# Optimization experiments

Hardware: AMD Instinct MI355X
Metric: run time of the kernel (lower is better)

## Reference

```python
import jax, jax.numpy as jnp
import numpy as np

N_NODES = 20000
N_EDGES = 640000
IN_DIM = 128
HID = 128
OUT_DIM = 3
N_GRAPHS = 32


def setup_inputs() -> dict:
    key = jax.random.key(0)
    ks = jax.random.split(key, 12)
    x = jax.random.normal(ks[0], (N_NODES, IN_DIM), dtype=jnp.float32)
    edge_index = jax.random.randint(ks[1], (2, N_EDGES), 0, N_NODES, dtype=jnp.int64)
    batch = jnp.sort(jax.random.randint(ks[2], (N_NODES,), 0, N_GRAPHS, dtype=jnp.int64))
    batch = batch.at[0].set(0).at[-1].set(N_GRAPHS - 1)
    s = 0.05
    W_gcn = jax.random.normal(ks[3], (IN_DIM, HID), jnp.float32) * s
    b_gcn = jnp.zeros((HID,), jnp.float32)
    W_sage_l = jax.random.normal(ks[4], (HID, HID), jnp.float32) * s  # neighbor branch
    W_sage_r = jax.random.normal(ks[5], (HID, HID), jnp.float32) * s  # root branch
    b_sage = jnp.zeros((HID,), jnp.float32)
    W_fc1 = jax.random.normal(ks[6], (HID, HID), jnp.float32) * s
    b_fc1 = jnp.zeros((HID,), jnp.float32)
    W_fc2 = jax.random.normal(ks[7], (HID, OUT_DIM), jnp.float32) * s
    b_fc2 = jnp.zeros((OUT_DIM,), jnp.float32)
    return {
        'x': x, 'edge_index': edge_index, 'batch': batch,
        'W_gcn': W_gcn, 'b_gcn': b_gcn,
        'W_sage_l': W_sage_l, 'W_sage_r': W_sage_r, 'b_sage': b_sage,
        'W_fc1': W_fc1, 'b_fc1': b_fc1, 'W_fc2': W_fc2, 'b_fc2': b_fc2,
    }


def reference(x, edge_index, batch, W_gcn, b_gcn, W_sage_l, W_sage_r, b_sage,
              W_fc1, b_fc1, W_fc2, b_fc2):
    n = x.shape[0]
    row, col = edge_index[0], edge_index[1]  # source -> target

    # ---- GCNConv: symmetric-normalized aggregation with self-loops ----
    h = x @ W_gcn  # [N, H]
    loops = jnp.arange(n, dtype=row.dtype)
    row_sl = jnp.concatenate([row, loops])
    col_sl = jnp.concatenate([col, loops])
    deg = jax.ops.segment_sum(jnp.ones_like(col_sl, dtype=h.dtype), col_sl,
                              num_segments=n)
    dinv = jnp.where(deg > 0, jax.lax.rsqrt(deg), 0.0)
    norm = dinv[row_sl] * dinv[col_sl]  # [E+N]
    h_gcn = jax.ops.segment_sum(h[row_sl] * norm[:, None], col_sl,
                                num_segments=n) + b_gcn
    h_gcn = jax.nn.relu(h_gcn)

    # ---- SAGEConv (mean aggregator) ----
    cnt = jax.ops.segment_sum(jnp.ones_like(col, dtype=h_gcn.dtype), col,
                              num_segments=n)
    neigh = jax.ops.segment_sum(h_gcn[row], col, num_segments=n)
    neigh = neigh / jnp.maximum(cnt, 1.0)[:, None]
    h_sage = neigh @ W_sage_l + h_gcn @ W_sage_r + b_sage
    h_sage = jax.nn.relu(h_sage)

    # ---- global_add_pool (num_graphs = 32 < 50) ----
    pooled = jax.ops.segment_sum(h_sage, batch, num_segments=N_GRAPHS)  # [G, H]

    # ---- MLP head ----
    out = jax.nn.relu(pooled @ W_fc1 + b_fc1) @ W_fc2 + b_fc2  # [G, 3]
    return out
```

## Files before the change

### kernel.cpp

```cpp
#include <hip/hip_runtime.h>

#define N_NODES 20000
#define N_EDGES 640000
#define HID 128
#define N_GRAPHS 32

#define SCAN_BLK 256
#define SCAN_NBLK ((N_NODES + SCAN_BLK - 1) / SCAN_BLK)

#define XT_STRIDE 36

__global__ __launch_bounds__(256) void hist_k(const int* __restrict__ col,
                                              int* __restrict__ cnt) {
    int e = blockIdx.x * blockDim.x + threadIdx.x;
    if (e < N_EDGES) {
        int c = col[e];
        if ((unsigned)c < N_NODES) atomicAdd(&cnt[c], 1);
    }
}

__global__ __launch_bounds__(SCAN_BLK) void scanA_k(const int* __restrict__ cnt,
                                                    int* __restrict__ blkSum) {
    __shared__ int wsum[SCAN_BLK / 64];
    const int b = blockIdx.x, t = threadIdx.x;
    const int i = b * SCAN_BLK + t;
    int v = (i < N_NODES) ? cnt[i] : 0;
#pragma unroll
    for (int o = 1; o < 64; o <<= 1) v += __shfl_xor(v, o);
    if ((t & 63) == 0) wsum[t >> 6] = v;
    __syncthreads();
    if (t == 0) {
        int s = 0;
#pragma unroll
        for (int w = 0; w < SCAN_BLK / 64; ++w) s += wsum[w];
        blkSum[b] = s;
    }
}

__global__ __launch_bounds__(SCAN_BLK) void scanB_k(const int* __restrict__ cnt,
                                                    const int* __restrict__ blkSum,
                                                    int* __restrict__ offs,
                                                    int* __restrict__ cursor,
                                                    float* __restrict__ dinv) {
    __shared__ int sm[SCAN_BLK];
    __shared__ int base_s;
    const int b = blockIdx.x, t = threadIdx.x;
    const int i = b * SCAN_BLK + t;
    const int v = (i < N_NODES) ? cnt[i] : 0;
    sm[t] = v;
    if (t == 0) {
        int s = 0;
        for (int k = 0; k < b; ++k) s += blkSum[k];
        base_s = s;
    }
    __syncthreads();
    for (int o = 1; o < SCAN_BLK; o <<= 1) {
        int add = (t >= o) ? sm[t - o] : 0;
        __syncthreads();
        sm[t] += add;
        __syncthreads();
    }
    if (i < N_NODES) {
        int excl = base_s + ((t > 0) ? sm[t - 1] : 0);
        offs[i] = excl;
        cursor[i] = excl;
        dinv[i] = rsqrtf((float)(v + 1));
        if (i == N_NODES - 1) offs[N_NODES] = excl + v;
    }
}

__global__ __launch_bounds__(256) void fill_k(const int* __restrict__ row,
                                              const int* __restrict__ col,
                                              int* __restrict__ cursor,
                                              int* __restrict__ csr_src) {
    int e = blockIdx.x * blockDim.x + threadIdx.x;
    if (e < N_EDGES) {
        int c = col[e];
        int r = row[e];
        if ((unsigned)c < N_NODES && (unsigned)r < N_NODES) {
            int p = atomicAdd(&cursor[c], 1);
            csr_src[p] = r;
        }
    }
}

__device__ __forceinline__ void stage_xt(float* xt, const float* __restrict__ Xm,
                                         int row0, int t) {
    const int r = t & 31;
    const int kbase = (t >> 5) * 16;
    const float* xp = Xm + (size_t)(row0 + r) * 128 + kbase;
#pragma unroll
    for (int c = 0; c < 4; ++c) {
        float4 v = *(const float4*)&xp[c * 4];
        xt[(kbase + c * 4 + 0) * XT_STRIDE + r] = v.x;
        xt[(kbase + c * 4 + 1) * XT_STRIDE + r] = v.y;
        xt[(kbase + c * 4 + 2) * XT_STRIDE + r] = v.z;
        xt[(kbase + c * 4 + 3) * XT_STRIDE + r] = v.w;
    }
}

__device__ __forceinline__ void gemm_half(const float* xt, const float* wbuf,
                                          int kb, int rg, int c4, float4 acc[4]) {
#pragma unroll 8
    for (int k0 = 0; k0 < 64; ++k0) {
        float4 w = *(const float4*)&wbuf[k0 * 128 + c4];
        float4 xr = *(const float4*)&xt[(kb + k0) * XT_STRIDE + rg * 4];
        acc[0].x = fmaf(xr.x, w.x, acc[0].x);
        acc[0].y = fmaf(xr.x, w.y, acc[0].y);
        acc[0].z = fmaf(xr.x, w.z, acc[0].z);
        acc[0].w = fmaf(xr.x, w.w, acc[0].w);
        acc[1].x = fmaf(xr.y, w.x, acc[1].x);
        acc[1].y = fmaf(xr.y, w.y, acc[1].y);
        acc[1].z = fmaf(xr.y, w.z, acc[1].z);
        acc[1].w = fmaf(xr.y, w.w, acc[1].w);
        acc[2].x = fmaf(xr.z, w.x, acc[2].x);
        acc[2].y = fmaf(xr.z, w.y, acc[2].y);
        acc[2].z = fmaf(xr.z, w.z, acc[2].z);
        acc[2].w = fmaf(xr.z, w.w, acc[2].w);
        acc[3].x = fmaf(xr.w, w.x, acc[3].x);
        acc[3].y = fmaf(xr.w, w.y, acc[3].y);
        acc[3].z = fmaf(xr.w, w.z, acc[3].z);
        acc[3].w = fmaf(xr.w, w.w, acc[3].w);
    }
}

__global__ __launch_bounds__(256) void gemm128_k(const float* __restrict__ X,
                                                 const float* __restrict__ W,
                                                 float* __restrict__ Y) {
    __shared__ float wbuf[64 * 128];
    __shared__ float xt[128 * XT_STRIDE];
    const int t = threadIdx.x;
    const int rg = t >> 5;
    const int c4 = (t & 31) * 4;
    const int row0 = blockIdx.x * 32;
    float4 acc[4];
    acc[0] = acc[1] = acc[2] = acc[3] = make_float4(0.f, 0.f, 0.f, 0.f);
    stage_xt(xt, X, row0, t);
#pragma unroll
    for (int kc = 0; kc < 2; ++kc) {
        if (kc) __syncthreads();
#pragma unroll
        for (int i = 0; i < 8; ++i)
            ((float4*)wbuf)[t + i * 256] = ((const float4*)W)[kc * 2048 + t + i * 256];
        __syncthreads();
        gemm_half(xt, wbuf, kc * 64, rg, c4, acc);
    }
#pragma unroll
    for (int i = 0; i < 4; ++i)
        *(float4*)&Y[(size_t)(row0 + rg * 4 + i) * 128 + c4] = acc[i];
}

__global__ __launch_bounds__(256) void gcn_agg_k(const float* __restrict__ h,
                                                 const int* __restrict__ offs,
                                                 const int* __restrict__ src,
                                                 const float* __restrict__ dinv,
                                                 const float* __restrict__ bias,
                                                 float* __restrict__ out) {
    const int wave = threadIdx.x >> 6;
    const int lane = threadIdx.x & 63;
    const int half = lane >> 5;
    const int node = (blockIdx.x * 4 + wave) * 2 + half;
    const int c4 = (lane & 31) * 4;
    const int nd = (node < N_NODES) ? node : (N_NODES - 1);
    const float dc = dinv[nd];
    float4 hv = *(const float4*)&h[(size_t)nd * 128 + c4];
    float4 acc = make_float4(dc * hv.x, dc * hv.y, dc * hv.z, dc * hv.w);
    const int beg = offs[nd];
    const int deg = offs[nd + 1] - beg;
    const int mdeg = max(deg, __shfl(deg, lane ^ 32));
    for (int j = 0; j < mdeg; j += 4) {
        int i0 = (j + 0 < deg) ? beg + j + 0 : 0;
        int i1 = (j + 1 < deg) ? beg + j + 1 : 0;
        int i2 = (j + 2 < deg) ? beg + j + 2 : 0;
        int i3 = (j + 3 < deg) ? beg + j + 3 : 0;
        int s0 = src[i0], s1 = src[i1], s2 = src[i2], s3 = src[i3];
        float w0 = (j + 0 < deg) ? dinv[s0] : 0.f;
        float w1 = (j + 1 < deg) ? dinv[s1] : 0.f;
        float w2 = (j + 2 < deg) ? dinv[s2] : 0.f;
        float w3 = (j + 3 < deg) ? dinv[s3] : 0.f;
        float4 v0 = *(const float4*)&h[(size_t)s0 * 128 + c4];
        float4 v1 = *(const float4*)&h[(size_t)s1 * 128 + c4];
        float4 v2 = *(const float4*)&h[(size_t)s2 * 128 + c4];
        float4 v3 = *(const float4*)&h[(size_t)s3 * 128 + c4];
        acc.x = fmaf(w0, v0.x, fmaf(w1, v1.x, fmaf(w2, v2.x, fmaf(w3, v3.x, acc.x))));
        acc.y = fmaf(w0, v0.y, fmaf(w1, v1.y, fmaf(w2, v2.y, fmaf(w3, v3.y, acc.y))));
        acc.z = fmaf(w0, v0.z, fmaf(w1, v1.z, fmaf(w2, v2.z, fmaf(w3, v3.z, acc.z))));
        acc.w = fmaf(w0, v0.w, fmaf(w1, v1.w, fmaf(w2, v2.w, fmaf(w3, v3.w, acc.w))));
    }
    float4 b = *(const float4*)&bias[c4];
    float4 o;
    o.x = fmaxf(fmaf(dc, acc.x, b.x), 0.f);
    o.y = fmaxf(fmaf(dc, acc.y, b.y), 0.f);
    o.z = fmaxf(fmaf(dc, acc.z, b.z), 0.f);
    o.w = fmaxf(fmaf(dc, acc.w, b.w), 0.f);
    if (node < N_NODES) *(float4*)&out[(size_t)node * 128 + c4] = o;
}

__global__ __launch_bounds__(256) void sage_agg_k(const float* __restrict__ hg,
                                                  const int* __restrict__ offs,
                                                  const int* __restrict__ src,
                                                  float* __restrict__ out) {
    const int wave = threadIdx.x >> 6;
    const int lane = threadIdx.x & 63;
    const int half = lane >> 5;
    const int node = (blockIdx.x * 4 + wave) * 2 + half;
    const int c4 = (lane & 31) * 4;
    const int nd = (node < N_NODES) ? node : (N_NODES - 1);
    float4 acc = make_float4(0.f, 0.f, 0.f, 0.f);
    const int beg = offs[nd];
    const int deg = offs[nd + 1] - beg;
    const int mdeg = max(deg, __shfl(deg, lane ^ 32));
    for (int j = 0; j < mdeg; j += 4) {
        int i0 = (j + 0 < deg) ? beg + j + 0 : 0;
        int i1 = (j + 1 < deg) ? beg + j + 1 : 0;
        int i2 = (j + 2 < deg) ? beg + j + 2 : 0;
        int i3 = (j + 3 < deg) ? beg + j + 3 : 0;
        float w0 = (j + 0 < deg) ? 1.f : 0.f;
        float w1 = (j + 1 < deg) ? 1.f : 0.f;
        float w2 = (j + 2 < deg) ? 1.f : 0.f;
        float w3 = (j + 3 < deg) ? 1.f : 0.f;
        int s0 = src[i0], s1 = src[i1], s2 = src[i2], s3 = src[i3];
        float4 v0 = *(const float4*)&hg[(size_t)s0 * 128 + c4];
        float4 v1 = *(const float4*)&hg[(size_t)s1 * 128 + c4];
        float4 v2 = *(const float4*)&hg[(size_t)s2 * 128 + c4];
        float4 v3 = *(const float4*)&hg[(size_t)s3 * 128 + c4];
        acc.x = fmaf(w0, v0.x, fmaf(w1, v1.x, fmaf(w2, v2.x, fmaf(w3, v3.x, acc.x))));
        acc.y = fmaf(w0, v0.y, fmaf(w1, v1.y, fmaf(w2, v2.y, fmaf(w3, v3.y, acc.y))));
        acc.z = fmaf(w0, v0.z, fmaf(w1, v1.z, fmaf(w2, v2.z, fmaf(w3, v3.z, acc.z))));
        acc.w = fmaf(w0, v0.w, fmaf(w1, v1.w, fmaf(w2, v2.w, fmaf(w3, v3.w, acc.w))));
    }
    float inv = 1.0f / (float)max(deg, 1);
    float4 o;
    o.x = acc.x * inv;
    o.y = acc.y * inv;
    o.z = acc.z * inv;
    o.w = acc.w * inv;
    if (node < N_NODES) *(float4*)&out[(size_t)node * 128 + c4] = o;
}

__global__ __launch_bounds__(256) void combine_k(const float* __restrict__ An,
                                                 const float* __restrict__ Bh,
                                                 const float* __restrict__ Wl,
                                                 const float* __restrict__ Wr,
                                                 const float* __restrict__ bias,
                                                 float* __restrict__ Y) {
    __shared__ float wbuf[64 * 128];
    __shared__ float xt[128 * XT_STRIDE];
    const int t = threadIdx.x;
    const int rg = t >> 5;
    const int c4 = (t & 31) * 4;
    const int row0 = blockIdx.x * 32;
    float4 acc[4];
    {
        float4 b = *(const float4*)&bias[c4];
        acc[0] = acc[1] = acc[2] = acc[3] = b;
    }
#pragma unroll
    for (int m = 0; m < 2; ++m) {
        const float* Wm = m ? Wr : Wl;
        const float* Xm = m ? Bh : An;
        if (m) __syncthreads();
        stage_xt(xt, Xm, row0, t);
#pragma unroll
        for (int kc = 0; kc < 2; ++kc) {
            if (m || kc) __syncthreads();
#pragma unroll
            for (int i = 0; i < 8; ++i)
                ((float4*)wbuf)[t + i * 256] = ((const float4*)Wm)[kc * 2048 + t + i * 256];
            __syncthreads();
            gemm_half(xt, wbuf, kc * 64, rg, c4, acc);
        }
    }
#pragma unroll
    for (int i = 0; i < 4; ++i) {
        float4 o = acc[i];
        o.x = fmaxf(o.x, 0.f);
        o.y = fmaxf(o.y, 0.f);
        o.z = fmaxf(o.z, 0.f);
        o.w = fmaxf(o.w, 0.f);
        *(float4*)&Y[(size_t)(row0 + rg * 4 + i) * 128 + c4] = o;
    }
}

#define POOL_ROWS 64
__global__ __launch_bounds__(256) void pool_k(const float* __restrict__ H,
                                              const int* __restrict__ batch,
                                              float* __restrict__ pooled) {
    const int r0 = blockIdx.x * POOL_ROWS;
    const int t = threadIdx.x;
    const int d = t & 127, half = t >> 7;
    const int rend = min(r0 + POOL_ROWS, N_NODES);
    int i = r0 + half;
    if (i >= rend) return;
    int cur = batch[i];
    float acc = 0.f;
    for (; i < rend; i += 2) {
        int g = batch[i];
        if (g != cur) {
            atomicAdd(&pooled[cur * 128 + d], acc);
            acc = 0.f;
            cur = g;
        }
        acc += H[(size_t)i * 128 + d];
    }
    atomicAdd(&pooled[cur * 128 + d], acc);
}

__global__ __launch_bounds__(128) void head_k(const float* __restrict__ pooled,
                                              const float* __restrict__ Wfc1,
                                              const float* __restrict__ bfc1,
                                              const float* __restrict__ Wfc2,
                                              const float* __restrict__ bfc2,
                                              float* __restrict__ out) {
    __shared__ float pl[128];
    __shared__ float tmp[128];
    const int g = blockIdx.x;
    const int t = threadIdx.x;
    pl[t] = pooled[g * 128 + t];
    __syncthreads();
    float a = bfc1[t];
#pragma unroll 8
    for (int k = 0; k < 128; ++k) a = fmaf(pl[k], Wfc1[k * 128 + t], a);
    tmp[t] = fmaxf(a, 0.f);
    __syncthreads();
    if (t < 3) {
        float a2 = bfc2[t];
        for (int k = 0; k < 128; ++k) a2 = fmaf(tmp[k], Wfc2[k * 3 + t], a2);
        out[g * 3 + t] = a2;
    }
}

extern "C" void kernel_launch(void* const* d_in, const int* in_sizes, int n_in,
                              void* d_out, int out_size, void* d_ws, size_t ws_size,
                              hipStream_t stream) {
    const float* x      = (const float*)d_in[0];
    const int*   ei     = (const int*)d_in[1];
    const int*   batch  = (const int*)d_in[2];
    const float* W_gcn  = (const float*)d_in[3];
    const float* b_gcn  = (const float*)d_in[4];
    const float* W_sl   = (const float*)d_in[5];
    const float* W_sr   = (const float*)d_in[6];
    const float* b_sage = (const float*)d_in[7];
    const float* W_fc1  = (const float*)d_in[8];
    const float* b_fc1  = (const float*)d_in[9];
    const float* W_fc2  = (const float*)d_in[10];
    const float* b_fc2  = (const float*)d_in[11];
    float* out = (float*)d_out;

    char* base = (char*)d_ws;
    size_t off = 0;
    auto take = [&](size_t bytes) -> void* {
        void* p = base + off;
        off += (bytes + 255) & ~(size_t)255;
        return p;
    };
    int*   cnt      = (int*)take((size_t)N_NODES * 4);
    int*   offs     = (int*)take((size_t)(N_NODES + 1) * 4);
    int*   cursor   = (int*)take((size_t)N_NODES * 4);
    float* dinv     = (float*)take((size_t)N_NODES * 4);
    int*   blkSum   = (int*)take((size_t)SCAN_NBLK * 4);
    int*   csr_src  = (int*)take((size_t)N_EDGES * 4);
    float* bufA     = (float*)take((size_t)N_NODES * HID * 4);
    float* bufB     = (float*)take((size_t)N_NODES * HID * 4);
    float* pooled   = (float*)take((size_t)N_GRAPHS * HID * 4);

    const int* row = ei;
    const int* col = ei + N_EDGES;

    hipMemsetAsync(cnt, 0, (size_t)N_NODES * 4, stream);
    hipMemsetAsync(pooled, 0, (size_t)N_GRAPHS * HID * 4, stream);

    hist_k<<<(N_EDGES + 255) / 256, 256, 0, stream>>>(col, cnt);
    scanA_k<<<SCAN_NBLK, SCAN_BLK, 0, stream>>>(cnt, blkSum);
    scanB_k<<<SCAN_NBLK, SCAN_BLK, 0, stream>>>(cnt, blkSum, offs, cursor, dinv);
    fill_k<<<(N_EDGES + 255) / 256, 256, 0, stream>>>(row, col, cursor, csr_src);

    const int gemm_blocks = N_NODES / 32;
    const int agg_blocks = (N_NODES + 7) / 8;
    gemm128_k<<<gemm_blocks, 256, 0, stream>>>(x, W_gcn, bufA);
    gcn_agg_k<<<agg_blocks, 256, 0, stream>>>(bufA, offs, csr_src, dinv, b_gcn, bufB);
    sage_agg_k<<<agg_blocks, 256, 0, stream>>>(bufB, offs, csr_src, bufA);
    combine_k<<<gemm_blocks, 256, 0, stream>>>(bufA, bufB, W_sl, W_sr, b_sage, bufA);
    pool_k<<<(N_NODES + POOL_ROWS - 1) / POOL_ROWS, 256, 0, stream>>>(bufA, batch, pooled);
    head_k<<<N_GRAPHS, 128, 0, stream>>>(pooled, W_fc1, b_fc1, W_fc2, b_fc2, out);
}
```

Before: 300.1 us.

## Fuse SAGE mean aggregation into combine GEMM via shared-memory staging

```diff
diff --git a/kernel.cpp b/kernel.cpp
--- a/kernel.cpp
+++ b/kernel.cpp
@@ -41,13 +41,19 @@
                                                     const int* __restrict__ blkSum,
                                                     int* __restrict__ offs,
                                                     int* __restrict__ cursor,
-                                                    float* __restrict__ dinv) {
+                                                    float* __restrict__ dinv,
+                                                    float* __restrict__ pooled) {
     __shared__ int sm[SCAN_BLK];
     __shared__ int base_s;
     const int b = blockIdx.x, t = threadIdx.x;
     const int i = b * SCAN_BLK + t;
     const int v = (i < N_NODES) ? cnt[i] : 0;
     sm[t] = v;
+    if (b == 0) {
+#pragma unroll
+        for (int j = 0; j < (N_GRAPHS * HID) / SCAN_BLK; ++j)
+            pooled[j * SCAN_BLK + t] = 0.f;
+    }
     if (t == 0) {
         int s = 0;
         for (int k = 0; k < b; ++k) s += blkSum[k];
@@ -196,79 +202,76 @@
     if (node < N_NODES) *(float4*)&out[(size_t)node * 128 + c4] = o;
 }
 
-__global__ __launch_bounds__(256) void sage_agg_k(const float* __restrict__ hg,
+__global__ __launch_bounds__(256) void fused_sc_k(const float* __restrict__ hg,
                                                   const int* __restrict__ offs,
                                                   const int* __restrict__ src,
-                                                  float* __restrict__ out) {
-    const int wave = threadIdx.x >> 6;
-    const int lane = threadIdx.x & 63;
-    const int half = lane >> 5;
-    const int node = (blockIdx.x * 4 + wave) * 2 + half;
-    const int c4 = (lane & 31) * 4;
-    const int nd = (node < N_NODES) ? node : (N_NODES - 1);
-    float4 acc = make_float4(0.f, 0.f, 0.f, 0.f);
-    const int beg = offs[nd];
-    const int deg = offs[nd + 1] - beg;
-    const int mdeg = max(deg, __shfl(deg, lane ^ 32));
-    for (int j = 0; j < mdeg; j += 4) {
-        int i0 = (j + 0 < deg) ? beg + j + 0 : 0;
-        int i1 = (j + 1 < deg) ? beg + j + 1 : 0;
-        int i2 = (j + 2 < deg) ? beg + j + 2 : 0;
-        int i3 = (j + 3 < deg) ? beg + j + 3 : 0;
-        float w0 = (j + 0 < deg) ? 1.f : 0.f;
-        float w1 = (j + 1 < deg) ? 1.f : 0.f;
-        float w2 = (j + 2 < deg) ? 1.f : 0.f;
-        float w3 = (j + 3 < deg) ? 1.f : 0.f;
-        int s0 = src[i0], s1 = src[i1], s2 = src[i2], s3 = src[i3];
-        float4 v0 = *(const float4*)&hg[(size_t)s0 * 128 + c4];
-        float4 v1 = *(const float4*)&hg[(size_t)s1 * 128 + c4];
-        float4 v2 = *(const float4*)&hg[(size_t)s2 * 128 + c4];
-        float4 v3 = *(const float4*)&hg[(size_t)s3 * 128 + c4];
-        acc.x = fmaf(w0, v0.x, fmaf(w1, v1.x, fmaf(w2, v2.x, fmaf(w3, v3.x, acc.x))));
-        acc.y = fmaf(w0, v0.y, fmaf(w1, v1.y, fmaf(w2, v2.y, fmaf(w3, v3.y, acc.y))));
-        acc.z = fmaf(w0, v0.z, fmaf(w1, v1.z, fmaf(w2, v2.z, fmaf(w3, v3.z, acc.z))));
-        acc.w = fmaf(w0, v0.w, fmaf(w1, v1.w, fmaf(w2, v2.w, fmaf(w3, v3.w, acc.w))));
-    }
-    float inv = 1.0f / (float)max(deg, 1);
-    float4 o;
-    o.x = acc.x * inv;
-    o.y = acc.y * inv;
-    o.z = acc.z * inv;
-    o.w = acc.w * inv;
-    if (node < N_NODES) *(float4*)&out[(size_t)node * 128 + c4] = o;
-}
-
-__global__ __launch_bounds__(256) void combine_k(const float* __restrict__ An,
-                                                 const float* __restrict__ Bh,
-                                                 const float* __restrict__ Wl,
-                                                 const float* __restrict__ Wr,
-                                                 const float* __restrict__ bias,
-                                                 float* __restrict__ Y) {
+                                                  const float* __restrict__ Wl,
+                                                  const float* __restrict__ Wr,
+                                                  const float* __restrict__ bias,
+                                                  float* __restrict__ Y) {
     __shared__ float wbuf[64 * 128];
     __shared__ float xt[128 * XT_STRIDE];
     const int t = threadIdx.x;
+    const int wave = t >> 6;
+    const int lane = t & 63;
+    const int half = lane >> 5;
+    const int c4 = (lane & 31) * 4;
+    const int row0 = blockIdx.x * 32;
+#pragma unroll
+    for (int p = 0; p < 4; ++p) {
+        const int nodeLocal = wave * 8 + p * 2 + half;
+        const int node = row0 + nodeLocal;
+        float4 acc = make_float4(0.f, 0.f, 0.f, 0.f);
+        const int beg = offs[node];
+        const int deg = offs[node + 1] - beg;
+        const int mdeg = max(deg, __shfl(deg, lane ^ 32));
+        for (int j = 0; j < mdeg; j += 4) {
+            int i0 = (j + 0 < deg) ? beg + j + 0 : 0;
+            int i1 = (j + 1 < deg) ? beg + j + 1 : 0;
+            int i2 = (j + 2 < deg) ? beg + j + 2 : 0;
+            int i3 = (j + 3 < deg) ? beg + j + 3 : 0;
+            float w0 = (j + 0 < deg) ? 1.f : 0.f;
+            float w1 = (j + 1 < deg) ? 1.f : 0.f;
+            float w2 = (j + 2 < deg) ? 1.f : 0.f;
+            float w3 = (j + 3 < deg) ? 1.f : 0.f;
+            int s0 = src[i0], s1 = src[i1], s2 = src[i2], s3 = src[i3];
+            float4 v0 = *(const float4*)&hg[(size_t)s0 * 128 + c4];
+            float4 v1 = *(const float4*)&hg[(size_t)s1 * 128 + c4];
+            float4 v2 = *(const float4*)&hg[(size_t)s2 * 128 + c4];
+            float4 v3 = *(const float4*)&hg[(size_t)s3 * 128 + c4];
+            acc.x = fmaf(w0, v0.x, fmaf(w1, v1.x, fmaf(w2, v2.x, fmaf(w3, v3.x, acc.x))));
+            acc.y = fmaf(w0, v0.y, fmaf(w1, v1.y, fmaf(w2, v2.y, fmaf(w3, v3.y, acc.y))));
+            acc.z = fmaf(w0, v0.z, fmaf(w1, v1.z, fmaf(w2, v2.z, fmaf(w3, v3.z, acc.z))));
+            acc.w = fmaf(w0, v0.w, fmaf(w1, v1.w, fmaf(w2, v2.w, fmaf(w3, v3.w, acc.w))));
+        }
+        const float inv = 1.0f / (float)max(deg, 1);
+        xt[(c4 + 0) * XT_STRIDE + nodeLocal] = acc.x * inv;
+        xt[(c4 + 1) * XT_STRIDE + nodeLocal] = acc.y * inv;
+        xt[(c4 + 2) * XT_STRIDE + nodeLocal] = acc.z * inv;
+        xt[(c4 + 3) * XT_STRIDE + nodeLocal] = acc.w * inv;
+    }
     const int rg = t >> 5;
-    const int c4 = (t & 31) * 4;
-    const int row0 = blockIdx.x * 32;
+    const int gc4 = (t & 31) * 4;
     float4 acc[4];
     {
-        float4 b = *(const float4*)&bias[c4];
+        float4 b = *(const float4*)&bias[gc4];
         acc[0] = acc[1] = acc[2] = acc[3] = b;
     }
 #pragma unroll
     for (int m = 0; m < 2; ++m) {
         const float* Wm = m ? Wr : Wl;
-        const float* Xm = m ? Bh : An;
-        if (m) __syncthreads();
-        stage_xt(xt, Xm, row0, t);
+        if (m) {
+            __syncthreads();
+            stage_xt(xt, hg, row0, t);
+        }
 #pragma unroll
         for (int kc = 0; kc < 2; ++kc) {
-            if (m || kc) __syncthreads();
+            __syncthreads();
 #pragma unroll
             for (int i = 0; i < 8; ++i)
                 ((float4*)wbuf)[t + i * 256] = ((const float4*)Wm)[kc * 2048 + t + i * 256];
             __syncthreads();
-            gemm_half(xt, wbuf, kc * 64, rg, c4, acc);
+            gemm_half(xt, wbuf, kc * 64, rg, gc4, acc);
         }
     }
 #pragma unroll
@@ -278,7 +281,7 @@
         o.y = fmaxf(o.y, 0.f);
         o.z = fmaxf(o.z, 0.f);
         o.w = fmaxf(o.w, 0.f);
-        *(float4*)&Y[(size_t)(row0 + rg * 4 + i) * 128 + c4] = o;
+        *(float4*)&Y[(size_t)(row0 + rg * 4 + i) * 128 + gc4] = o;
     }
 }
 
@@ -368,19 +371,18 @@
     const int* col = ei + N_EDGES;
 
     hipMemsetAsync(cnt, 0, (size_t)N_NODES * 4, stream);
-    hipMemsetAsync(pooled, 0, (size_t)N_GRAPHS * HID * 4, stream);
 
     hist_k<<<(N_EDGES + 255) / 256, 256, 0, stream>>>(col, cnt);
     scanA_k<<<SCAN_NBLK, SCAN_BLK, 0, stream>>>(cnt, blkSum);
-    scanB_k<<<SCAN_NBLK, SCAN_BLK, 0, stream>>>(cnt, blkSum, offs, cursor, dinv);
+    scanB_k<<<SCAN_NBLK, SCAN_BLK, 0, stream>>>(cnt, blkSum, offs, cursor, dinv, pooled);
     fill_k<<<(N_EDGES + 255) / 256, 256, 0, stream>>>(row, col, cursor, csr_src);
 
     const int gemm_blocks = N_NODES / 32;
     const int agg_blocks = (N_NODES + 7) / 8;
     gemm128_k<<<gemm_blocks, 256, 0, stream>>>(x, W_gcn, bufA);
     gcn_agg_k<<<agg_blocks, 256, 0, stream>>>(bufA, offs, csr_src, dinv, b_gcn, bufB);
-    sage_agg_k<<<agg_blocks, 256, 0, stream>>>(bufB, offs, csr_src, bufA);
-    combine_k<<<gemm_blocks, 256, 0, stream>>>(bufA, bufB, W_sl, W_sr, b_sage, bufA);
+    fused_sc_k<<<gemm_blocks, 256, 0, stream>>>(bufB, offs, csr_src, W_sl, W_sr,
+                                                b_sage, bufA);
     pool_k<<<(N_NODES + POOL_ROWS - 1) / POOL_ROWS, 256, 0, stream>>>(bufA, batch, pooled);
     head_k<<<N_GRAPHS, 128, 0, stream>>>(pooled, W_fc1, b_fc1, W_fc2, b_fc2, out);
 }
```

Measured after the change: 294.5 us. No clear change (-1.9%).
